# Kernel tuning notes

Measured on AMD Instinct MI355X. Metric: run time of the kernel, lower is better.

The kernel has to match this reference:

```python
import jax, jax.numpy as jnp
import numpy as np

B, S, D_MODEL = 2, 2048, 2048
N_HEADS, N_KV = 32, 8
HEAD_DIM = D_MODEL // N_HEADS          # 64
HPG = N_HEADS // N_KV                  # heads per group = 4
DIM_K = HEAD_DIM * N_KV                # 512 (used as softmax scale per original code)


def setup_inputs() -> dict:
    key = jax.random.key(0)
    ks = jax.random.split(key, 11)
    s = lambda fan_in: 1.0 / np.sqrt(fan_in)
    return {
        "inputs_q": jax.random.normal(ks[0], (B, S, D_MODEL), jnp.float32),
        "inputs_k": jax.random.normal(ks[1], (B, S, D_MODEL), jnp.float32),
        "inputs_v": jax.random.normal(ks[2], (B, S, D_MODEL), jnp.float32),
        "Wq": jax.random.normal(ks[3], (D_MODEL, D_MODEL), jnp.float32) * s(D_MODEL),
        "bq": jnp.zeros((D_MODEL,), jnp.float32),
        "Wk": jax.random.normal(ks[4], (D_MODEL, DIM_K), jnp.float32) * s(D_MODEL),
        "bk": jnp.zeros((DIM_K,), jnp.float32),
        "Wv": jax.random.normal(ks[5], (D_MODEL, DIM_K), jnp.float32) * s(D_MODEL),
        "bv": jnp.zeros((DIM_K,), jnp.float32),
        "Wo": jax.random.normal(ks[6], (D_MODEL, D_MODEL), jnp.float32) * s(D_MODEL),
        "bo": jnp.zeros((D_MODEL,), jnp.float32),
    }


def reference(inputs_q, inputs_k, inputs_v, Wq, bq, Wk, bk, Wv, bv, Wo, bo):
    b, s, _ = inputs_q.shape
    q = inputs_q @ Wq + bq                       # [B,S,dim_q]
    k = inputs_k @ Wk + bk                       # [B,S,dim_k]
    v = inputs_v @ Wv + bv                       # [B,S,dim_v]
    q = q.reshape(b, s, N_KV, HPG, HEAD_DIM)     # b m g p d
    k = k.reshape(b, s, N_KV, HEAD_DIM)          # b n g d
    v = v.reshape(b, s, N_KV, HEAD_DIM)          # b n g d
    # logits[b,g,p,m,n] = q . k ; scale by sqrt(dim_k) per original code
    logits = jnp.einsum('bmgpd,bngd->bgpmn', q, k) / jnp.sqrt(jnp.float32(DIM_K))
    # causal mask (lower triangular allowed)
    causal = jnp.tril(jnp.ones((s, s), bool))
    logits = jnp.where(causal, logits, -jnp.inf)
    attn = jax.nn.softmax(logits, axis=-1)       # [B,G,P,M,N]
    out = jnp.einsum('bgpmn,bngd->bmgpd', attn, v)
    out = out.reshape(b, s, N_KV * HPG * HEAD_DIM)
    return out @ Wo + bo
```

## Files before the change

kernel.cpp:

```cpp
#include <hip/hip_runtime.h>
#include <hip/hip_bf16.h>

typedef __hip_bfloat16 bf16;
typedef float f32x4 __attribute__((ext_vector_type(4)));
typedef float f32x16 __attribute__((ext_vector_type(16)));
typedef short bf16x8 __attribute__((ext_vector_type(8)));

#define B_   2
#define S_   2048
#define DM   2048
#define HD   64
#define NH   32

__device__ __forceinline__ void async16(void* lds, const void* g) {
  __builtin_amdgcn_global_load_lds(
      (const __attribute__((address_space(1))) unsigned int*)g,
      (__attribute__((address_space(3))) unsigned int*)lds, 16, 0, 0);
}

template <int N> __device__ __forceinline__ void waitvm() {
  asm volatile("s_waitcnt vmcnt(%0)" :: "i"(N) : "memory");
}

__device__ __forceinline__ float exp2a(float x) {
  float r; asm("v_exp_f32 %0, %1" : "=v"(r) : "v"(x)); return r;
}
__device__ __forceinline__ unsigned cvtpk(float lo, float hi) {
  unsigned r; asm("v_cvt_pk_bf16_f32 %0, %1, %2" : "=v"(r) : "v"(lo), "v"(hi)); return r;
}
__device__ __forceinline__ void perm32swap(unsigned &a, unsigned &b) {
  asm volatile("v_permlane32_swap_b32 %0, %1" : "+v"(a), "+v"(b));
}

__global__ __launch_bounds__(256)
void prep_kernel(const float* __restrict__ xq, const float* __restrict__ xk,
                 const float* __restrict__ xv,
                 const float* __restrict__ Wq, const float* __restrict__ Wo,
                 const float* __restrict__ Wk, const float* __restrict__ Wv,
                 const float* __restrict__ bk, const float* __restrict__ bv,
                 bf16* __restrict__ Xq, bf16* __restrict__ Xk, bf16* __restrict__ Xv,
                 bf16* __restrict__ WqT, bf16* __restrict__ WoT, bf16* __restrict__ WkvT,
                 float* __restrict__ bkv) {
  const int blk = blockIdx.x;
  const int tid = threadIdx.x;

  if (blk < 12288) {
    const int a = blk >> 12;
    const int r = blk & 4095;
    const float* in = (a == 0) ? xq : (a == 1) ? xk : xv;
    bf16* out = (a == 0) ? Xq : (a == 1) ? Xk : Xv;
    const size_t i = ((size_t)r * 256 + tid) * 8;
    float4 v0 = *(const float4*)(in + i);
    float4 v1 = *(const float4*)(in + i + 4);
    union { bf16 h[8]; uint4 v; } u;
    u.h[0] = __float2bfloat16(v0.x); u.h[1] = __float2bfloat16(v0.y);
    u.h[2] = __float2bfloat16(v0.z); u.h[3] = __float2bfloat16(v0.w);
    u.h[4] = __float2bfloat16(v1.x); u.h[5] = __float2bfloat16(v1.y);
    u.h[6] = __float2bfloat16(v1.z); u.h[7] = __float2bfloat16(v1.w);
    *(uint4*)(out + i) = u.v;
    return;
  }

  int t = blk - 12288;
  const float* W; bf16* Wt; int N;
  if (t < 2048)       { W = Wq; Wt = WqT; N = 2048; }
  else if (t < 4096)  { t -= 2048; W = Wo; Wt = WoT; N = 2048; }
  else if (t < 4608)  { t -= 4096; W = Wk; Wt = WkvT; N = 512; }
  else if (t < 5120)  { t -= 4608; W = Wv; Wt = WkvT + (size_t)512 * 2048; N = 512; }
  else {
    #pragma unroll
    for (int j = 0; j < 4; ++j) {
      const int i = tid * 4 + j;
      bkv[i] = (i < 512) ? bk[i] : bv[i - 512];
    }
    return;
  }
  const int k0 = (t & 63) * 32, n0 = (t >> 6) * 64;
  __shared__ float tile[32][65];
  const int tx = tid & 63, ty = tid >> 6;
  #pragma unroll
  for (int i = 0; i < 32; i += 4)
    tile[ty + i][tx] = W[(size_t)(k0 + ty + i) * N + n0 + tx];
  __syncthreads();
  const int nl = tid >> 2, kc = (tid & 3) * 8;
  union { bf16 h[8]; uint4 v; } u;
  #pragma unroll
  for (int j = 0; j < 8; ++j)
    u.h[j] = __float2bfloat16(tile[kc + j][nl]);
  *(uint4*)(Wt + (size_t)(n0 + nl) * 2048 + k0 + kc) = u.v;
}

__device__ __forceinline__ void store_out(float* C, size_t idx, float v) { C[idx] = v; }
__device__ __forceinline__ void store_out(bf16* C, size_t idx, float v) { C[idx] = __float2bfloat16(v); }

template <typename OUT>
__device__ __forceinline__ void gemm_body(const bf16* __restrict__ Au,
                                          const bf16* __restrict__ Bt,
                                          const float* __restrict__ bias, float omul,
                                          OUT* __restrict__ C, int N, int m0, int n0,
                                          bf16* As, bf16* Bs) {
  constexpr int BK = 32;
  const int tid = threadIdx.x;
  const int wave = tid >> 6, lane = tid & 63;
  const int l15 = lane & 15, l4 = lane >> 4;
  const int wm = (wave & 1) * 64, wn = (wave >> 1) * 64;

  f32x4 acc[4][4] = {};
  const int nk = 2048 / BK;

  auto stage = [&](int kt, int buf) {
    const int k0 = kt * BK;
    #pragma unroll
    for (int i = 0; i < 2; ++i) {
      const int rb = wave * 32 + i * 16;
      const int r  = rb + (lane >> 2);
      const int cs = (lane & 3) ^ ((r >> 1) & 3);
      async16(As + buf * 4096 + rb * BK, Au + (size_t)(m0 + r) * 2048 + k0 + cs * 8);
      async16(Bs + buf * 4096 + rb * BK, Bt + (size_t)(n0 + r) * 2048 + k0 + cs * 8);
    }
  };

  stage(0, 0);
  asm volatile("s_waitcnt vmcnt(0)" ::: "memory");
  __syncthreads();

  for (int kt = 0; kt < nk; ++kt) {
    const int cur = kt & 1;
    if (kt + 1 < nk) stage(kt + 1, cur ^ 1);
    bf16x8 af[4], bfr[4];
    #pragma unroll
    for (int f = 0; f < 4; ++f) {
      const int mr = wm + f * 16 + l15;
      af[f]  = *(const bf16x8*)(As + cur * 4096 + mr * BK + (l4 ^ ((mr >> 1) & 3)) * 8);
      const int nr = wn + f * 16 + l15;
      bfr[f] = *(const bf16x8*)(Bs + cur * 4096 + nr * BK + (l4 ^ ((nr >> 1) & 3)) * 8);
    }
    __builtin_amdgcn_s_setprio(1);
    #pragma unroll
    for (int i = 0; i < 4; ++i)
      #pragma unroll
      for (int j = 0; j < 4; ++j)
        acc[i][j] = __builtin_amdgcn_mfma_f32_16x16x32_bf16(af[i], bfr[j], acc[i][j], 0, 0, 0);
    __builtin_amdgcn_s_setprio(0);
    asm volatile("s_waitcnt vmcnt(0)" ::: "memory");
    __syncthreads();
  }

  const int r0 = m0 + wm + l4 * 4;
  const int c0 = n0 + wn + l15;
  #pragma unroll
  for (int j = 0; j < 4; ++j) {
    const int col = c0 + j * 16;
    const float bb = bias[col];
    #pragma unroll
    for (int i = 0; i < 4; ++i)
      #pragma unroll
      for (int r = 0; r < 4; ++r)
        store_out(C, (size_t)(r0 + i * 16 + r) * N + col, (acc[i][j][r] + bb) * omul);
  }
}

__device__ __forceinline__ void gemm256_body(const bf16* __restrict__ Au,
                                             const bf16* __restrict__ Bt,
                                             const float* __restrict__ bias, float omul,
                                             bf16* __restrict__ C, int N, int m0, int n0,
                                             char* smem) {
  char* AsB = smem;
  char* BsB = smem + 65536;
  const int tid = threadIdx.x;
  const int wave = tid >> 6, lane = tid & 63;
  const int l15 = lane & 15, l4 = lane >> 4;
  const int wr = wave >> 2, wc = wave & 3;

  f32x4 acc[8][4] = {};

  auto stage = [&](int buf, int kt) {
    const int k0 = kt * 64;
    #pragma unroll
    for (int i = 0; i < 4; ++i) {
      const int rb = wave * 32 + i * 8;
      const int r = rb + (lane >> 3);
      const int cs = (lane & 7) ^ (r & 7);
      async16(AsB + buf * 32768 + rb * 128, Au + (size_t)(m0 + r) * 2048 + k0 + cs * 8);
      async16(BsB + buf * 32768 + rb * 128, Bt + (size_t)(n0 + r) * 2048 + k0 + cs * 8);
    }
  };

  stage(0, 0);
  waitvm<0>();
  __builtin_amdgcn_s_barrier();
  asm volatile("" ::: "memory");

  for (int kt = 0; kt < 32; ++kt) {
    const int cur = kt & 1;
    if (kt + 1 < 32) stage(cur ^ 1, kt + 1);
    const char* ab = AsB + cur * 32768;
    const char* bb = BsB + cur * 32768;
    #pragma unroll
    for (int ks = 0; ks < 2; ++ks) {
      bf16x8 af[8], bg[4];
      #pragma unroll
      for (int mf = 0; mf < 8; ++mf) {
        const int row = wr * 128 + mf * 16 + l15;
        af[mf] = *(const bf16x8*)(ab + row * 128 + (((ks * 4 + l4) ^ (row & 7)) << 4));
      }
      #pragma unroll
      for (int nf = 0; nf < 4; ++nf) {
        const int row = wc * 64 + nf * 16 + l15;
        bg[nf] = *(const bf16x8*)(bb + row * 128 + (((ks * 4 + l4) ^ (row & 7)) << 4));
      }
      __builtin_amdgcn_s_setprio(1);
      #pragma unroll
      for (int mf = 0; mf < 8; ++mf)
        #pragma unroll
        for (int nf = 0; nf < 4; ++nf)
          acc[mf][nf] = __builtin_amdgcn_mfma_f32_16x16x32_bf16(af[mf], bg[nf],
                                                                acc[mf][nf], 0, 0, 0);
      __builtin_amdgcn_s_setprio(0);
    }
    waitvm<0>();
    __builtin_amdgcn_s_barrier();
    asm volatile("" ::: "memory");
  }

  const int r0 = m0 + wr * 128 + l4 * 4;
  const int c0 = n0 + wc * 64 + l15;
  #pragma unroll
  for (int nf = 0; nf < 4; ++nf) {
    const int col = c0 + nf * 16;
    const float bb2 = bias[col];
    #pragma unroll
    for (int mf = 0; mf < 8; ++mf)
      #pragma unroll
      for (int r = 0; r < 4; ++r)
        C[(size_t)(r0 + mf * 16 + r) * N + col] =
            __float2bfloat16((acc[mf][nf][r] + bb2) * omul);
  }
}

__global__ __launch_bounds__(512, 2)
void gemm_qkv(const bf16* __restrict__ Xq, const bf16* __restrict__ Xk,
              const bf16* __restrict__ Xv,
              const bf16* __restrict__ WqT, const bf16* __restrict__ WkvT,
              const float* __restrict__ bq, const float* __restrict__ bkv,
              bf16* __restrict__ Qb, bf16* __restrict__ KVb) {
  __shared__ __align__(16) char smem[131072];
  const int bid = blockIdx.x;
  const int wgid = (bid & 7) * 24 + (bid >> 3);
  const int m0 = (wgid & 15) * 256;
  const int ng = wgid >> 4;
  if (ng < 8) {
    gemm256_body(Xq, WqT, bq, 0.063758717f, Qb, 2048, m0, ng * 256, smem);
  } else {
    const int n0 = (ng - 8) * 256;
    gemm256_body(n0 < 512 ? Xk : Xv, WkvT, bkv, 1.0f, KVb, 1024, m0, n0, smem);
  }
}

__global__ __launch_bounds__(256)
void gemm_o(const bf16* __restrict__ AO, const bf16* __restrict__ WoT,
            const float* __restrict__ bo, float* __restrict__ out) {
  __shared__ __align__(16) bf16 As[2][128 * 32];
  __shared__ __align__(16) bf16 Bs[2][128 * 32];
  const int xcd = blockIdx.x & 7, i = blockIdx.x >> 3;
  const int n = xcd * 2 + (i >> 5);
  const int m = i & 31;
  gemm_body<float>(AO, WoT, bo, 1.0f, out, 2048,
                   m * 128, n * 128, &As[0][0], &Bs[0][0]);
}

__global__ __launch_bounds__(256, 3)
void attn_kernel(const bf16* __restrict__ Q, const bf16* __restrict__ KV, bf16* __restrict__ O) {
  const int bi = blockIdx.x;
  const int w = bi >> 8, c = bi & 255;
  const int grp = c >> 6, hb = c & 63;
  int qt;
  if (w == 0)      qt = 15 - grp;
  else if (w == 1) qt = 8 + grp;
  else if (w == 2) qt = 7 - grp;
  else             qt = grp;
  const int h = hb & 31, b = hb >> 5;
  const int g = h >> 2;
  const int tid = threadIdx.x;
  const int wave = tid >> 6, lane = tid & 63;
  const int l31 = lane & 31, l5 = lane >> 5;

  __shared__ __align__(16) char smem[40960];
  bf16* KsBuf = (bf16*)smem;
  bf16* VtBuf = (bf16*)(smem + 24576);
  char* ob = smem + wave * 4608;

  const bf16* KVb = KV + (size_t)(b * S_) * 1024;
  const int kcol = g * HD;
  const int vcol = 512 + g * HD;
  const int kv2 = tid & 31, vd0 = (tid >> 5) * 8;

  auto stageK = [&](int buf, int kv0) {
    #pragma unroll
    for (int i2 = 0; i2 < 2; ++i2) {
      const int rb = wave * 16 + i2 * 8;
      const int r = rb + (lane >> 3);
      const int cs = (lane & 7) ^ (r & 7);
      async16(KsBuf + buf * 4096 + rb * 64, KVb + (size_t)(kv0 + r) * 1024 + kcol + cs * 8);
    }
  };
  auto writeV = [&](int buf, uint4 va, uint4 vb) {
    const unsigned short* a0 = (const unsigned short*)&va;
    const unsigned short* a1 = (const unsigned short*)&vb;
    char* base = (char*)VtBuf + buf * 8192;
    #pragma unroll
    for (int j = 0; j < 8; ++j) {
      unsigned val = (unsigned)a0[j] | ((unsigned)a1[j] << 16);
      const int d = vd0 + j;
      *(unsigned*)(base + d * 128 + ((kv2 * 4) ^ ((d & 7) << 4))) = val;
    }
  };

  const int qbase = qt * 128;
  const int nt = 2 * qt + 2;
  const int qrow = qbase + wave * 32 + l31;
  const int wmax = qbase + wave * 32 + 31;

  bf16x8 qf[4];
  const bf16* qp = Q + (size_t)(b * S_ + qrow) * DM + h * HD + l5 * 8;
  #pragma unroll
  for (int ks = 0; ks < 4; ++ks) qf[ks] = *(const bf16x8*)(qp + ks * 16);

  union { unsigned u[4]; bf16x8 v; } ones;
  {
    const unsigned ov = (l31 == 0) ? 0x3F803F80u : 0u;
    ones.u[0] = ov; ones.u[1] = ov; ones.u[2] = ov; ones.u[3] = ov;
  }

  f32x16 ot[2] = {};
  f32x16 ot2 = {};
  uint4 vr0, vr1;

  {
    const bf16* vp = KVb + (size_t)(2 * kv2) * 1024 + vcol + vd0;
    vr0 = *(const uint4*)vp;
    vr1 = *(const uint4*)(vp + 1024);
  }
  stageK(0, 0);
  stageK(1, 64);
  waitvm<4>();
  writeV(0, vr0, vr1);
  waitvm<2>();
  asm volatile("s_waitcnt lgkmcnt(0)" ::: "memory");
  __builtin_amdgcn_s_barrier();
  asm volatile("" ::: "memory");

  for (int t = 0; t < nt; ++t) {
    const int kv0 = t * 64;
    if (t + 1 < nt) {
      const bf16* vp = KVb + (size_t)((t + 1) * 64 + 2 * kv2) * 1024 + vcol + vd0;
      vr0 = *(const uint4*)vp;
      vr1 = *(const uint4*)(vp + 1024);
    }
    if (t + 2 < nt) stageK((t + 2) % 3, (t + 2) * 64);

    if (kv0 <= wmax) {
      const char* kb = (const char*)(KsBuf + (t % 3) * 4096);
      const char* vb = (const char*)(VtBuf + (t & 1) * 4096);
      f32x16 sT[2] = {};
      __builtin_amdgcn_s_setprio(1);
      #pragma unroll
      for (int ks = 0; ks < 4; ++ks) {
        #pragma unroll
        for (int i = 0; i < 2; ++i) {
          const int row = i * 32 + l31;
          bf16x8 kf = *(const bf16x8*)(kb + row * 128 +
                                       ((ks * 32 + l5 * 16) ^ ((row & 7) << 4)));
          sT[i] = __builtin_amdgcn_mfma_f32_32x32x16_bf16(kf, qf[ks], sT[i], 0, 0, 0);
        }
      }
      __builtin_amdgcn_s_setprio(0);
      if (kv0 + 63 > qbase + wave * 32) {
        #pragma unroll
        for (int i = 0; i < 2; ++i)
          #pragma unroll
          for (int r = 0; r < 16; ++r) {
            const int kvg = kv0 + i * 32 + ((r & 3) + 8 * (r >> 2)) + 4 * l5;
            if (kvg > qrow) sT[i][r] = -3.0e38f;
          }
      }
      unsigned pk[2][8];
      #pragma unroll
      for (int i = 0; i < 2; ++i)
        #pragma unroll
        for (int rr = 0; rr < 8; ++rr) {
          const float p0 = exp2a(sT[i][2 * rr]);
          const float p1 = exp2a(sT[i][2 * rr + 1]);
          pk[i][rr] = cvtpk(p0, p1);
        }
      #pragma unroll
      for (int i = 0; i < 2; ++i) {
        #pragma unroll
        for (int kp = 0; kp < 2; ++kp) {
          unsigned w0 = pk[i][4 * kp + 0], w1 = pk[i][4 * kp + 1];
          unsigned w2 = pk[i][4 * kp + 2], w3 = pk[i][4 * kp + 3];
          perm32swap(w0, w2);
          perm32swap(w1, w3);
          union { unsigned u[4]; bf16x8 v; } pf = {{w0, w1, w2, w3}};
          const int ks2 = i * 2 + kp;
          __builtin_amdgcn_s_setprio(1);
          #pragma unroll
          for (int f = 0; f < 2; ++f) {
            const int row = f * 32 + l31;
            bf16x8 vf = *(const bf16x8*)(vb + row * 128 +
                                         ((ks2 * 32 + l5 * 16) ^ ((row & 7) << 4)));
            ot[f] = __builtin_amdgcn_mfma_f32_32x32x16_bf16(vf, pf.v, ot[f], 0, 0, 0);
          }
          ot2 = __builtin_amdgcn_mfma_f32_32x32x16_bf16(ones.v, pf.v, ot2, 0, 0, 0);
          __builtin_amdgcn_s_setprio(0);
        }
      }
    }

    if (t + 2 < nt) waitvm<2>();
    else            waitvm<0>();
    if (t + 1 < nt) writeV((t + 1) & 1, vr0, vr1);
    asm volatile("s_waitcnt lgkmcnt(0)" ::: "memory");
    __builtin_amdgcn_s_barrier();
    asm volatile("" ::: "memory");
  }

  const float lsum = ot2[0] + __shfl_xor(ot2[0], 32);
  const float inv = 1.0f / lsum;
  #pragma unroll
  for (int f = 0; f < 2; ++f)
    #pragma unroll
    for (int g2 = 0; g2 < 4; ++g2) {
      uint2 val;
      val.x = cvtpk(ot[f][g2 * 4 + 0] * inv, ot[f][g2 * 4 + 1] * inv);
      val.y = cvtpk(ot[f][g2 * 4 + 2] * inv, ot[f][g2 * 4 + 3] * inv);
      *(uint2*)(ob + l31 * 144 + f * 64 + g2 * 16 + l5 * 8) = val;
    }
  asm volatile("s_waitcnt lgkmcnt(0)" ::: "memory");
  __builtin_amdgcn_sched_barrier(0);
  #pragma unroll
  for (int rr = 0; rr < 4; ++rr) {
    const int row = rr * 8 + (lane >> 3);
    uint4 dv = *(const uint4*)(ob + row * 144 + (lane & 7) * 16);
    *(uint4*)(O + (size_t)(b * S_ + qbase + wave * 32 + row) * DM + h * HD + (lane & 7) * 8) = dv;
  }
}

extern "C" void kernel_launch(void* const* d_in, const int* in_sizes, int n_in,
                              void* d_out, int out_size, void* d_ws, size_t ws_size,
                              hipStream_t stream) {
  const float* xq = (const float*)d_in[0];
  const float* xk = (const float*)d_in[1];
  const float* xv = (const float*)d_in[2];
  const float* Wq = (const float*)d_in[3];
  const float* bq = (const float*)d_in[4];
  const float* Wk = (const float*)d_in[5];
  const float* bk = (const float*)d_in[6];
  const float* Wv = (const float*)d_in[7];
  const float* bv = (const float*)d_in[8];
  const float* Wo = (const float*)d_in[9];
  const float* bo = (const float*)d_in[10];
  float* out = (float*)d_out;

  char* ws = (char*)d_ws;
  bf16*  Xq   = (bf16*)(ws);
  bf16*  Xk   = (bf16*)(ws + 16777216);
  bf16*  Xv   = (bf16*)(ws + 33554432);
  bf16*  WqT  = (bf16*)(ws + 50331648);
  bf16*  WkvT = (bf16*)(ws + 58720256);
  bf16*  WoT  = (bf16*)(ws + 62914560);
  float* bkv  = (float*)(ws + 71303168);
  bf16*  Qb   = (bf16*)(ws + 71307264);
  bf16*  KVb  = (bf16*)(ws + 88084480);
  bf16*  AO   = Xq;

  prep_kernel<<<17409, 256, 0, stream>>>(xq, xk, xv, Wq, Wo, Wk, Wv, bk, bv,
                                         Xq, Xk, Xv, WqT, WoT, WkvT, bkv);
  gemm_qkv<<<192, 512, 0, stream>>>(Xq, Xk, Xv, WqT, WkvT, bq, bkv, Qb, KVb);
  attn_kernel<<<1024, 256, 0, stream>>>(Qb, KVb, AO);
  gemm_o<<<512, 256, 0, stream>>>(AO, WoT, bo, out);
}
```

Baseline: 203.8 us.

## Pipeline QKV GEMM at half-K granularity with finer-grained async loads

Replaces the double-buffered 64-wide K staging in the QKV projection GEMM with four 32-wide half-tile slots per operand. Loads for the next and next-next K steps are issued in between four compute phases per iteration, gated by partial vmcnt waits. The aim is to keep global-to-LDS traffic in flight across MFMA phases instead of draining all loads at each iteration end. It adds two barriers per phase and relies on the vmcnt counts matching the issue order, which is fragile.

```diff
diff --git a/kernel.cpp b/kernel.cpp
--- a/kernel.cpp
+++ b/kernel.cpp
@@ -160,11 +160,11 @@
   }
 }
 
-__device__ __forceinline__ void gemm256_body(const bf16* __restrict__ Au,
-                                             const bf16* __restrict__ Bt,
-                                             const float* __restrict__ bias, float omul,
-                                             bf16* __restrict__ C, int N, int m0, int n0,
-                                             char* smem) {
+__device__ __forceinline__ void gemm256_8p(const bf16* __restrict__ Au,
+                                           const bf16* __restrict__ Bt,
+                                           const float* __restrict__ bias, float omul,
+                                           bf16* __restrict__ C, int N, int m0, int n0,
+                                           char* smem) {
   char* AsB = smem;
   char* BsB = smem + 65536;
   const int tid = threadIdx.x;
@@ -173,54 +173,65 @@
   const int wr = wave >> 2, wc = wave & 3;
 
   f32x4 acc[8][4] = {};
-
-  auto stage = [&](int buf, int kt) {
-    const int k0 = kt * 64;
-    #pragma unroll
-    for (int i = 0; i < 4; ++i) {
-      const int rb = wave * 32 + i * 8;
-      const int r = rb + (lane >> 3);
-      const int cs = (lane & 7) ^ (r & 7);
-      async16(AsB + buf * 32768 + rb * 128, Au + (size_t)(m0 + r) * 2048 + k0 + cs * 8);
-      async16(BsB + buf * 32768 + rb * 128, Bt + (size_t)(n0 + r) * 2048 + k0 + cs * 8);
+  const bf16* As = Au + (size_t)m0 * 2048;
+  const bf16* Bs = Bt + (size_t)n0 * 2048;
+
+  auto stageH = [&](const bf16* src, char* region, int kt, int kh) {
+    const int k0 = kt * 64 + kh * 32;
+    char* slot = region + (kh * 2 + (kt & 1)) * 16384;
+    #pragma unroll
+    for (int i = 0; i < 2; ++i) {
+      const int rb = wave * 32 + i * 16;
+      const int r = rb + (lane >> 2);
+      const int cs = (lane & 3) ^ ((r >> 1) & 3);
+      async16(slot + rb * 64, src + (size_t)r * 2048 + k0 + cs * 8);
     }
   };
 
-  stage(0, 0);
+  stageH(As, AsB, 0, 0); stageH(Bs, BsB, 0, 0);
+  stageH(As, AsB, 0, 1); stageH(Bs, BsB, 0, 1);
   waitvm<0>();
   __builtin_amdgcn_s_barrier();
-  asm volatile("" ::: "memory");
-
-  for (int kt = 0; kt < 32; ++kt) {
-    const int cur = kt & 1;
-    if (kt + 1 < 32) stage(cur ^ 1, kt + 1);
-    const char* ab = AsB + cur * 32768;
-    const char* bb = BsB + cur * 32768;
-    #pragma unroll
-    for (int ks = 0; ks < 2; ++ks) {
-      bf16x8 af[8], bg[4];
-      #pragma unroll
-      for (int mf = 0; mf < 8; ++mf) {
-        const int row = wr * 128 + mf * 16 + l15;
-        af[mf] = *(const bf16x8*)(ab + row * 128 + (((ks * 4 + l4) ^ (row & 7)) << 4));
+  stageH(Bs, BsB, 1, 0); stageH(As, AsB, 1, 0); stageH(Bs, BsB, 1, 1);
+
+  bf16x8 bg[4];
+  const int nk = 32;
+  for (int T = 0; T < nk; ++T) {
+    const int par = T & 1;
+    #pragma unroll
+    for (int q = 0; q < 4; ++q) {
+      waitvm<6>();
+      const int kk = q >> 1, mh = q & 1;
+      const char* aslot = AsB + (kk * 2 + par) * 16384;
+      const char* bslot = BsB + (kk * 2 + par) * 16384;
+      bf16x8 af[4];
+      #pragma unroll
+      for (int m2 = 0; m2 < 4; ++m2) {
+        const int row = wr * 128 + (mh * 4 + m2) * 16 + l15;
+        af[m2] = *(const bf16x8*)(aslot + row * 64 + ((l4 ^ ((row >> 1) & 3)) << 4));
       }
-      #pragma unroll
-      for (int nf = 0; nf < 4; ++nf) {
-        const int row = wc * 64 + nf * 16 + l15;
-        bg[nf] = *(const bf16x8*)(bb + row * 128 + (((ks * 4 + l4) ^ (row & 7)) << 4));
+      if (mh == 0) {
+        #pragma unroll
+        for (int nf = 0; nf < 4; ++nf) {
+          const int row = wc * 64 + nf * 16 + l15;
+          bg[nf] = *(const bf16x8*)(bslot + row * 64 + ((l4 ^ ((row >> 1) & 3)) << 4));
+        }
       }
+      if (q == 0)      { if (T + 1 < nk) stageH(As, AsB, T + 1, 1); }
+      else if (q == 1) { if (T + 2 < nk) stageH(Bs, BsB, T + 2, 0); }
+      else if (q == 2) { if (T + 2 < nk) stageH(As, AsB, T + 2, 0); }
+      else             { if (T + 2 < nk) stageH(Bs, BsB, T + 2, 1); }
+      __builtin_amdgcn_s_barrier();
       __builtin_amdgcn_s_setprio(1);
       #pragma unroll
-      for (int mf = 0; mf < 8; ++mf)
+      for (int m2 = 0; m2 < 4; ++m2)
         #pragma unroll
         for (int nf = 0; nf < 4; ++nf)
-          acc[mf][nf] = __builtin_amdgcn_mfma_f32_16x16x32_bf16(af[mf], bg[nf],
-                                                                acc[mf][nf], 0, 0, 0);
+          acc[mh * 4 + m2][nf] = __builtin_amdgcn_mfma_f32_16x16x32_bf16(
+              af[m2], bg[nf], acc[mh * 4 + m2][nf], 0, 0, 0);
       __builtin_amdgcn_s_setprio(0);
-    }
-    waitvm<0>();
-    __builtin_amdgcn_s_barrier();
-    asm volatile("" ::: "memory");
+      __builtin_amdgcn_s_barrier();
+    }
   }
 
   const int r0 = m0 + wr * 128 + l4 * 4;
@@ -250,10 +261,10 @@
   const int m0 = (wgid & 15) * 256;
   const int ng = wgid >> 4;
   if (ng < 8) {
-    gemm256_body(Xq, WqT, bq, 0.063758717f, Qb, 2048, m0, ng * 256, smem);
+    gemm256_8p(Xq, WqT, bq, 0.063758717f, Qb, 2048, m0, ng * 256, smem);
   } else {
     const int n0 = (ng - 8) * 256;
-    gemm256_body(n0 < 512 ? Xk : Xv, WkvT, bkv, 1.0f, KVb, 1024, m0, n0, smem);
+    gemm256_8p(n0 < 512 ? Xk : Xv, WkvT, bkv, 1.0f, KVb, 1024, m0, n0, smem);
   }
 }
 
```

Result: no change. 204.7 us (+0.4%).
